# Kernel optimization log

Hardware: AMD Instinct MI355X
Metric: run time of the kernel (lower is better)

Reference implementation:

```python
import jax, jax.numpy as jnp
import numpy as np


def _conv(x, w, b, pad_h=0):
    # x: [B,C,H,W_feat], w: [O,C,kh,1]; kernel width is 1 so this is a 1D conv along H
    y = jax.lax.conv_general_dilated(
        x, w, window_strides=(1, 1), padding=[(pad_h, pad_h), (0, 0)],
        dimension_numbers=('NCHW', 'OIHW', 'NCHW'))
    return y + b[None, :, None, None]


def _lin(x, w, b):
    # Semi_Linear: shared nn.Linear applied to the last axis of every [channel, height] slice.
    # Since the nested loops cover the full leading dims, this is one batched matmul.
    return jnp.einsum('bchi,oi->bcho', x, w) + b


def setup_inputs() -> dict:
    key = jax.random.key(0)
    ks = jax.random.split(key, 40)
    B = 4096
    rn = lambda k, shape, s=0.1: jax.random.normal(k, shape, jnp.float32) * s
    d = {}
    d['x'] = jax.random.normal(ks[0], (B, 1, 5, 127), jnp.float32)
    # block A params (first set of definitions in __init__)
    d['ca1_w'] = rn(ks[1], (5, 1, 3, 1));    d['ca1_b'] = rn(ks[2], (5,))
    d['l01_w'] = rn(ks[3], (81, 127));        d['l01_b'] = rn(ks[4], (81,))
    d['cb1_w'] = rn(ks[5], (25, 5, 3, 1));    d['cb1_b'] = rn(ks[6], (25,))
    d['cc1_w'] = rn(ks[7], (25, 1, 1, 1));    d['cc1_b'] = rn(ks[8], (25,))
    d['r01_w'] = rn(ks[9], (81, 127));        d['r01_b'] = rn(ks[10], (81,))
    # block B params
    d['c1_w'] = rn(ks[11], (75, 25, 2, 1));   d['c1_b'] = rn(ks[12], (75,))
    d['l1_w'] = rn(ks[13], (30, 81));         d['l1_b'] = rn(ks[14], (30,))
    d['c2_w'] = rn(ks[15], (125, 75, 2, 1));  d['c2_b'] = rn(ks[16], (125,))
    d['ca_w'] = rn(ks[17], (125, 25, 3, 1));  d['ca_b'] = rn(ks[18], (125,))
    d['ra_w'] = rn(ks[19], (30, 81));         d['ra_b'] = rn(ks[20], (30,))
    # block C params (second, overriding set of definitions)
    d['ca2_w'] = rn(ks[21], (25, 125, 2, 1)); d['ca2_b'] = rn(ks[22], (25,))
    d['l02_w'] = rn(ks[23], (10, 30));        d['l02_b'] = rn(ks[24], (10,))
    d['cb2_w'] = rn(ks[25], (1, 25, 2, 1));   d['cb2_b'] = rn(ks[26], (1,))
    d['cc2_w'] = rn(ks[27], (1, 125, 1, 1));  d['cc2_b'] = rn(ks[28], (1,))
    d['r02_w'] = rn(ks[29], (10, 30));        d['r02_b'] = rn(ks[30], (10,))
    d['fl_w'] = rn(ks[31], (1, 10));          d['fl_b'] = rn(ks[32], (1,))
    return d


def reference(x, ca1_w, ca1_b, l01_w, l01_b, cb1_w, cb1_b, cc1_w, cc1_b, r01_w, r01_b,
              c1_w, c1_b, l1_w, l1_b, c2_w, c2_b, ca_w, ca_b, ra_w, ra_b,
              ca2_w, ca2_b, l02_w, l02_b, cb2_w, cb2_b, cc2_w, cc2_b, r02_w, r02_b,
              fl_w, fl_b):
    # block A
    z = _conv(x, ca1_w, ca1_b, pad_h=1)            # [B,5,5,127]
    z = jax.nn.relu(_lin(z, l01_w, l01_b))         # [B,5,5,81]
    z = _conv(z, cb1_w, cb1_b, pad_h=1)            # [B,25,5,81]
    y = _lin(x, r01_w, r01_b)                      # [B,1,5,81]
    y = _conv(y, cc1_w, cc1_b)                     # [B,25,5,81]
    x1 = z + y
    # block B
    z = _conv(x1, c1_w, c1_b)                      # [B,75,4,81]
    z = jax.nn.relu(_lin(z, l1_w, l1_b))           # [B,75,4,30]
    z = _conv(z, c2_w, c2_b)                       # [B,125,3,30]
    y = _lin(x1, ra_w, ra_b)                       # [B,25,5,30]
    y = _conv(y, ca_w, ca_b)                       # [B,125,3,30]
    x2 = z + y
    # block C
    z = _conv(x2, ca2_w, ca2_b)                    # [B,25,2,30]
    z = jax.nn.relu(_lin(z, l02_w, l02_b))         # [B,25,2,10]
    z = _conv(z, cb2_w, cb2_b)                     # [B,1,1,10]
    y = _lin(x2, r02_w, r02_b)                     # [B,125,3,10]
    y = _conv(y, cc2_w, cc2_b)                     # [B,1,3,10]
    x3 = z + y                                     # broadcast -> [B,1,3,10]
    return _lin(x3, fl_w, fl_b)                    # [B,1,3,1]
```

## Files before the change

### kernel.cpp

```cpp
#include <hip/hip_runtime.h>


typedef unsigned short u16;
typedef __attribute__((ext_vector_type(8))) short bf16x8;
typedef __attribute__((ext_vector_type(4))) float f32x4;
typedef __attribute__((ext_vector_type(8))) unsigned short u16x8;
typedef __attribute__((ext_vector_type(2))) unsigned int u32x2;

__device__ __forceinline__ float bf2f(u16 u) {
  return __uint_as_float(((unsigned)u) << 16);
}
__device__ __forceinline__ u16 f2bf(float f) {
  unsigned u = __float_as_uint(f);
  return (u16)((u + 0x7FFFu + ((u >> 16) & 1u)) >> 16);
}

#define Z4 make_float4(0.f, 0.f, 0.f, 0.f)

#define OF_CS01   0
#define OF_CS1    81
#define OF_CSR    111
#define OF_CSAC   141
#define OF_CS02   266
#define OF_CSCC2  276
#define OF_L01T   280
#define OF_R01T   10948
#define OF_SWT    21616
#define OF_CB1T   26800
#define OF_C1T    27175
#define OF_SCT    30928
#define OF_CA2T   31528
#define OF_WT2    41528
#define OF_ZPAD   57912
#define OF_C1W2   57920
#define F32_TOTAL 60480

#define R_XT   0
#define R_XL   635
#define R_YA   1040
#define R_ZA   1445
#define R_P    3470
#define R_Q    4970
#define R_VLP  5270
#define R_VRP  12770
#define R_TP   16520
#define R_X2   0
#define R_XJ   12770
#define ROWS_TOTAL 25520

struct Ctx {
  const float *x, *ca1_w, *ca1_b, *l01_b, *r01_b, *cb1_b, *cc1_w, *cc1_b;
  const float *c1_b, *l1_b, *c2_b, *ca_b, *ra_b, *ca2_b, *l02_b;
  const float *cb2_w, *cb2_b, *cc2_w, *cc2_b, *r02_b, *fl_w, *fl_b;
  const float *l01_w, *r01_w, *l1_w, *ra_w, *c1_w, *c2_w, *ca_w, *cb1_w;
  const float *l02_w, *r02_w, *ca2_w;
  float *F;
  float *zAcc;
  float *yAcc;
  u16 *A;
  float *out;
  int CB;
  int b0g;
};

__global__ __launch_bounds__(256) void k0c(Ctx C) {
  const int t0 = blockIdx.x * 256 + threadIdx.x;
  const int NT = 32 * 256;
  float* F = C.F;
  for (int k = t0; k < 277; k += NT) {
    float s = 0.f;
    if (k < 81)       { for (int i = 0; i < 127; ++i) s += C.l01_w[k * 127 + i]; F[OF_CS01 + k] = s; }
    else if (k < 111) { int j = k - 81;  for (int a = 0; a < 81; ++a) s += C.l1_w[j * 81 + a]; F[OF_CS1 + j] = s; }
    else if (k < 141) { int j = k - 111; for (int a = 0; a < 81; ++a) s += C.ra_w[j * 81 + a]; F[OF_CSR + j] = s; }
    else if (k < 266) { int o = k - 141; for (int i = 0; i < 75; ++i) s += C.ca_w[o * 75 + i]; F[OF_CSAC + o] = s; }
    else if (k < 276) { int q = k - 266; for (int j = 0; j < 30; ++j) s += C.l02_w[q * 30 + j]; F[OF_CS02 + q] = s; }
    else              { float ss = 0.f; for (int o = 0; o < 125; ++o) ss += C.cc2_w[o]; F[OF_CSCC2] = ss; }
  }
  for (int e = t0; e < 8; e += NT) F[OF_ZPAD + e] = 0.f;
  for (int e = t0; e < 10668; e += NT) { int i = e / 84, a = e % 84;
    F[OF_L01T + e] = (a < 81) ? C.l01_w[a * 127 + i] : 0.f; }
  for (int e = t0; e < 10668; e += NT) { int i = e / 84, a = e % 84;
    F[OF_R01T + e] = (a < 81) ? C.r01_w[a * 127 + i] : 0.f; }
  for (int e = t0; e < 5184; e += NT)  { int a = e / 64, j2 = e % 64;
    F[OF_SWT + e] = (j2 < 30) ? C.l1_w[j2 * 81 + a]
                  : (j2 < 60) ? C.ra_w[(j2 - 30) * 81 + a] : 0.f; }
  for (int e = t0; e < 375; e += NT)   { int k = e / 25, c = e % 25; F[OF_CB1T + e] = C.cb1_w[c * 15 + k]; }
  for (int e = t0; e < 600; e += NT)   { int j = e / 20, q2 = e % 20;
    F[OF_SCT + e] = (q2 < 10) ? C.l02_w[q2 * 30 + j] : C.r02_w[(q2 - 10) * 30 + j]; }
  for (int e = t0; e < 10000; e += NT) { int k = e / 40, r = e % 40, cg = r / 8, i = r % 8;
    F[OF_CA2T + e] = (i < 5) ? C.ca2_w[(cg * 5 + i) * 250 + k] : 0.f; }
  u16* WT2 = (u16*)(F + OF_WT2);
  for (int e = t0; e < 32768; e += NT) {
    int o = e >> 8, k = e & 255;
    float v = 0.f;
    if (o < 125) {
      if (k < 150) v = C.c2_w[o * 150 + k];
      else if (k >= 160 && k < 235) v = C.ca_w[o * 75 + (k - 160)];
    }
    WT2[e] = f2bf(v);
  }
  u16* C1W2 = (u16*)(F + OF_C1W2);
  for (int e = t0; e < 5120; e += NT) {
    int o = e >> 6, k = e & 63;
    float v = (o < 75 && k < 50) ? C.c1_w[o * 50 + k] : 0.f;
    C1W2[e] = f2bf(v);
  }
}

__global__ __launch_bounds__(256) void k0t(Ctx C) {
  __shared__ float tile[64][65];
  const int tid = threadIdx.x;
  const int b0 = blockIdx.x * 64;
  const int i0 = blockIdx.y * 64;
  for (int e = tid; e < 64 * 64; e += 256) {
    int s = e >> 6, ii = e & 63, gi = i0 + ii;
    if (gi < 635) tile[s][ii] = C.x[(size_t)(C.b0g + b0 + s) * 635 + gi];
  }
  __syncthreads();
  const int lane = tid & 63, wv = tid >> 6;
  u16* xT = C.A + (size_t)R_XT * C.CB;
#pragma unroll
  for (int k = 0; k < 16; ++k) {
    int r = wv * 16 + k, gi = i0 + r;
    if (gi < 635) xT[(size_t)gi * C.CB + b0 + lane] = f2bf(tile[lane][r]);
  }
}

__global__ __launch_bounds__(256) void k1(Ctx C) {
  const int col = blockIdx.x * 256 + threadIdx.x;
  if (col >= C.CB) return;
  const int g = blockIdx.y, type = g / 15, r = g % 15, h = r / 3, a0 = (r % 3) * 28;
  const size_t cb = (size_t)C.CB;
  const u16* __restrict__ xT = C.A + (size_t)R_XT * cb;
  const float* __restrict__ wT = C.F + (type ? OF_R01T : OF_L01T) + a0;
  float4 A0=Z4,A1=Z4,A2=Z4,A3=Z4,A4=Z4,A5=Z4,A6=Z4;
  for (int i = 0; i < 127; ++i) {
    float xv = bf2f(xT[(size_t)(h * 127 + i) * cb + col]);
    const float4* __restrict__ W = (const float4*)(wT + i * 84);
#define K1F(Aq, P) { float4 w = W[P]; Aq.x += w.x*xv; Aq.y += w.y*xv; Aq.z += w.z*xv; Aq.w += w.w*xv; }
    K1F(A0,0) K1F(A1,1) K1F(A2,2) K1F(A3,3) K1F(A4,4) K1F(A5,5) K1F(A6,6)
#undef K1F
  }
  u16* dst = C.A + (size_t)(type ? R_YA : R_XL) * cb;
  auto wr = [&](int a, float v) {
    if (a < 81) {
      float rr = v + (type ? C.r01_b[a] : 0.f);
      dst[(size_t)(h * 81 + a) * cb + col] = f2bf(rr);
    }
  };
#define K1O(Aq, P) { wr(a0+4*P+0, Aq.x); wr(a0+4*P+1, Aq.y); wr(a0+4*P+2, Aq.z); wr(a0+4*P+3, Aq.w); }
  K1O(A0,0) K1O(A1,1) K1O(A2,2) K1O(A3,3) K1O(A4,4) K1O(A5,5) K1O(A6,6)
#undef K1O
}

__global__ __launch_bounds__(256) void k2(Ctx C) {
  const int col = blockIdx.x * 256 + threadIdx.x;
  if (col >= C.CB) return;
  const int g = blockIdx.y, c5 = g / 15, r = g % 15, h = r / 3, a0 = (r % 3) * 27;
  const u16* __restrict__ XL = C.A + (size_t)R_XL * C.CB;
  const float* __restrict__ F = C.F;
  float acc[27];
  float cb = C.ca1_b[c5];
#pragma unroll
  for (int a = 0; a < 27; ++a) acc[a] = cb * F[OF_CS01 + a0 + a] + C.l01_b[a0 + a];
#pragma unroll
  for (int dh = 0; dh < 3; ++dh) {
    int hp = h - 1 + dh;
    if (hp < 0 || hp > 4) continue;
    float w = C.ca1_w[c5 * 3 + dh];
#pragma unroll
    for (int a = 0; a < 27; ++a) acc[a] += w * bf2f(XL[(size_t)(hp * 81 + a0 + a) * C.CB + col]);
  }
  u16* zA = C.A + (size_t)R_ZA * C.CB;
#pragma unroll
  for (int a = 0; a < 27; ++a)
    zA[(size_t)((c5 * 5 + h) * 81 + a0 + a) * C.CB + col] = f2bf(fmaxf(acc[a], 0.f));
}

__global__ __launch_bounds__(256) void k3(Ctx C) {
  const int col = blockIdx.x * 256 + threadIdx.x;
  if (col >= C.CB) return;
  const int g = blockIdx.y, pair = g >> 1, j0 = (g & 1) * 32;
  const bool isP = (pair < 25);
  const size_t cb = (size_t)C.CB;
  const u16* __restrict__ src = C.A + (size_t)(isP ? (R_ZA + pair * 81) : (R_YA + (pair - 25) * 81)) * cb;
  const float* __restrict__ SWT = C.F + OF_SWT + j0;
  float4 A0=Z4,A1=Z4,A2=Z4,A3=Z4,A4=Z4,A5=Z4,A6=Z4,A7=Z4;
  for (int a = 0; a < 81; ++a) {
    float xv = bf2f(src[(size_t)a * cb + col]);
    const float4* __restrict__ W = (const float4*)(SWT + a * 64);
#define K3F(Aq, P) { float4 w = W[P]; Aq.x += w.x*xv; Aq.y += w.y*xv; Aq.z += w.z*xv; Aq.w += w.w*xv; }
    K3F(A0,0) K3F(A1,1) K3F(A2,2) K3F(A3,3) K3F(A4,4) K3F(A5,5) K3F(A6,6) K3F(A7,7)
#undef K3F
  }
  u16* dst = C.A + (size_t)(isP ? (R_P + pair * 60) : (R_Q + (pair - 25) * 60)) * cb;
  auto wr = [&](int j2, float v) {
    if (j2 < 60) dst[(size_t)j2 * cb + col] = f2bf(v);
  };
#define K3O(Aq, P) { wr(j0+4*P+0, Aq.x); wr(j0+4*P+1, Aq.y); wr(j0+4*P+2, Aq.z); wr(j0+4*P+3, Aq.w); }
  K3O(A0,0) K3O(A1,1) K3O(A2,2) K3O(A3,3) K3O(A4,4) K3O(A5,5) K3O(A6,6) K3O(A7,7)
#undef K3O
}

__global__ __launch_bounds__(256) void k4(Ctx C) {
  const int col = blockIdx.x * 256 + threadIdx.x;
  if (col >= C.CB) return;
  const int g = blockIdx.y, cg = g / 60, j2 = g % 60;
  const size_t cb = (size_t)C.CB;
  const u16* __restrict__ Pb = C.A + (size_t)R_P * cb;
  const u16* __restrict__ Qb = C.A + (size_t)R_Q * cb;
  const float* __restrict__ F = C.F;
  float sj = (j2 < 30) ? F[OF_CS1 + j2] : F[OF_CSR + (j2 - 30)];
  float acc[5][5];
#pragma unroll
  for (int cl = 0; cl < 5; ++cl) {
    int c = cg * 5 + cl;
    float base = (C.cb1_b[c] + C.cc1_b[c]) * sj;
    float cw = C.cc1_w[c];
#pragma unroll
    for (int h = 0; h < 5; ++h)
      acc[cl][h] = base + cw * bf2f(Qb[(size_t)(h * 60 + j2) * cb + col]);
  }
#pragma unroll
  for (int c5 = 0; c5 < 5; ++c5)
#pragma unroll
    for (int hp = 0; hp < 5; ++hp) {
      float pv = bf2f(Pb[(size_t)((c5 * 5 + hp) * 60 + j2) * cb + col]);
#pragma unroll
      for (int dh = 0; dh < 3; ++dh) {
        int h = hp + 1 - dh;
        if (h < 0 || h > 4) continue;
        const float* __restrict__ w = F + OF_CB1T + (c5 * 3 + dh) * 25 + cg * 5;
#pragma unroll
        for (int cl = 0; cl < 5; ++cl) acc[cl][h] += w[cl] * pv;
      }
    }
  if (j2 < 30) {
    u16* vlp = C.A + (size_t)R_VLP * cb;
#pragma unroll
    for (int cl = 0; cl < 5; ++cl) {
      int base = (cg * 5 + cl) * 30 + j2;
#pragma unroll
      for (int h = 0; h < 5; ++h)
        vlp[(size_t)(base + h * 750) * cb + col] = f2bf(acc[cl][h]);
    }
  } else {
    u16* vrp = C.A + (size_t)R_VRP * cb;
    int jr = j2 - 30;
#pragma unroll
    for (int cl = 0; cl < 5; ++cl) {
      int base = (cg * 5 + cl) * 30 + jr;
#pragma unroll
      for (int h = 0; h < 5; ++h)
        vrp[(size_t)(base + h * 750) * cb + col] = f2bf(acc[cl][h]);
    }
  }
}

union CvtAF { u32x2 p[2]; bf16x8 v; };

__global__ __launch_bounds__(256, 2) void k5m(Ctx C) {
  __shared__ u16 sA[8192];
  const int tid = threadIdx.x;
  const int col0 = blockIdx.x * 128;
  const int gy = blockIdx.y;
  const int j = gy >> 2, h4 = gy & 3;
  const size_t cb = (size_t)C.CB;
  const u16* __restrict__ A_ = C.A;
  const u16* __restrict__ WB = (const u16*)(C.F + OF_C1W2);
  const float* __restrict__ F = C.F;

  const int x = tid & 63, wv = tid >> 6;
  const int klane = (x >> 1) & 3;
  const int m0s = ((x >> 3) << 4) + ((x & 1) << 3);
  const u16* zsrc = (const u16*)(F + OF_ZPAD);
#pragma unroll
  for (int p = 0; p < 4; ++p) {
    int k = p * 16 + wv * 4 + klane;
    const u16* src;
    if (k >= 50) {
      src = zsrc;
    } else {
      int c = k >> 1, dc = k & 1;
      int srow = R_VLP + (h4 + dc) * 750 + c * 30 + j;
      src = A_ + (size_t)srow * cb + col0 + m0s;
    }
    __builtin_amdgcn_global_load_lds(
        (const __attribute__((address_space(1))) void*)src,
        (__attribute__((address_space(3))) void*)&sA[(p * 4 + wv) * 512],
        16, 0, 0);
  }

  const int l = tid & 63, w = tid >> 6;
  const int lc = l & 15, q = l >> 4;
#define BF(N, S) (*(const bf16x8*)(WB + (size_t)((N)*16 + lc) * 64 + (S)*32 + q*8))
  bf16x8 B00 = BF(0,0), B10 = BF(1,0), B20 = BF(2,0), B30 = BF(3,0), B40 = BF(4,0);
  bf16x8 B01 = BF(0,1), B11 = BF(1,1), B21 = BF(2,1), B31 = BF(3,1), B41 = BF(4,1);
#undef BF
  float s1 = F[OF_CS1 + j], lb = C.l1_b[j];
  const int o4r = 64 + lc;
  const int o4c = (o4r < 75) ? o4r : 0;
  float bs0 = C.c1_b[lc] * s1 + lb;
  float bs1 = C.c1_b[16 + lc] * s1 + lb;
  float bs2 = C.c1_b[32 + lc] * s1 + lb;
  float bs3 = C.c1_b[48 + lc] * s1 + lb;
  float bs4 = C.c1_b[o4c] * s1 + lb;

  __syncthreads();

  unsigned ldsbase = (unsigned)(size_t)(&sA[0]);
  unsigned ta = ldsbase + (unsigned)((2 * q) * 1024 + w * 256 + lc * 8);

  u32x2 e00,e01,e02,e03, e10,e11,e12,e13;
  asm volatile("ds_read_b64_tr_b16 %0, %1"             : "=&v"(e00) : "v"(ta));
  asm volatile("ds_read_b64_tr_b16 %0, %1 offset:1024" : "=&v"(e01) : "v"(ta));
  asm volatile("ds_read_b64_tr_b16 %0, %1 offset:8192" : "=&v"(e02) : "v"(ta));
  asm volatile("ds_read_b64_tr_b16 %0, %1 offset:9216" : "=&v"(e03) : "v"(ta));
  asm volatile("ds_read_b64_tr_b16 %0, %1 offset:128"  : "=&v"(e10) : "v"(ta));
  asm volatile("ds_read_b64_tr_b16 %0, %1 offset:1152" : "=&v"(e11) : "v"(ta));
  asm volatile("ds_read_b64_tr_b16 %0, %1 offset:8320" : "=&v"(e12) : "v"(ta));
  asm volatile("ds_read_b64_tr_b16 %0, %1 offset:9344" : "=&v"(e13) : "v"(ta));
  asm volatile("s_waitcnt lgkmcnt(0)" ::: "memory");
  __builtin_amdgcn_sched_barrier(0);

  bf16x8 f0s0, f0s1, f1s0, f1s1;
  { CvtAF c_; c_.p[0]=e00; c_.p[1]=e01; f0s0=c_.v; }
  { CvtAF c_; c_.p[0]=e02; c_.p[1]=e03; f0s1=c_.v; }
  { CvtAF c_; c_.p[0]=e10; c_.p[1]=e11; f1s0=c_.v; }
  { CvtAF c_; c_.p[0]=e12; c_.p[1]=e13; f1s1=c_.v; }

  f32x4 a00={0,0,0,0},a01={0,0,0,0},a02={0,0,0,0},a03={0,0,0,0},a04={0,0,0,0};
  f32x4 a10={0,0,0,0},a11={0,0,0,0},a12={0,0,0,0},a13={0,0,0,0},a14={0,0,0,0};
#define MF(AC, FA, BB) AC = __builtin_amdgcn_mfma_f32_16x16x32_bf16(FA, BB, AC, 0, 0, 0);
  MF(a00,f0s0,B00) MF(a01,f0s0,B10) MF(a02,f0s0,B20) MF(a03,f0s0,B30) MF(a04,f0s0,B40)
  MF(a10,f1s0,B00) MF(a11,f1s0,B10) MF(a12,f1s0,B20) MF(a13,f1s0,B30) MF(a14,f1s0,B40)
  MF(a00,f0s1,B01) MF(a01,f0s1,B11) MF(a02,f0s1,B21) MF(a03,f0s1,B31) MF(a04,f0s1,B41)
  MF(a10,f1s1,B01) MF(a11,f1s1,B11) MF(a12,f1s1,B21) MF(a13,f1s1,B31) MF(a14,f1s1,B41)
#undef MF

  u16* tp = C.A + (size_t)R_TP * cb;
  const int cw0 = col0 + 2 * w * 16 + q * 4;
#define ST(AC, O, BS, CW) { int o_ = (O); if (o_ < 75) { \
    size_t rw = (size_t)(h4 * 2250 + o_ * 30 + j) * cb + (CW); \
    ushort4 pk; pk.x = f2bf(fmaxf(AC[0]+(BS),0.f)); pk.y = f2bf(fmaxf(AC[1]+(BS),0.f)); \
    pk.z = f2bf(fmaxf(AC[2]+(BS),0.f)); pk.w = f2bf(fmaxf(AC[3]+(BS),0.f)); \
    *(ushort4*)(tp + rw) = pk; } }
  ST(a00, lc,      bs0, cw0)      ST(a01, 16 + lc, bs1, cw0)
  ST(a02, 32 + lc, bs2, cw0)      ST(a03, 48 + lc, bs3, cw0)
  ST(a04, 64 + lc, bs4, cw0)
  ST(a10, lc,      bs0, cw0 + 16) ST(a11, 16 + lc, bs1, cw0 + 16)
  ST(a12, 32 + lc, bs2, cw0 + 16) ST(a13, 48 + lc, bs3, cw0 + 16)
  ST(a14, 64 + lc, bs4, cw0 + 16)
#undef ST
}

#define RD(D, TA, OFF) asm volatile("ds_read_b64_tr_b16 %0, %1 offset:" OFF : "=&v"(D) : "v"(TA));
#define TRS_EVEN(TA) \
  RD(p00,TA,"0")     RD(p01,TA,"1024")  RD(p10,TA,"8192")  RD(p11,TA,"9216") \
  RD(p20,TA,"16384") RD(p21,TA,"17408") RD(p30,TA,"24576") RD(p31,TA,"25600") \
  RD(p40,TA,"32768") RD(p41,TA,"33792") RD(p50,TA,"40960") RD(p51,TA,"41984") \
  RD(p60,TA,"49152") RD(p61,TA,"50176") RD(p70,TA,"57344") RD(p71,TA,"58368")
#define TRS_ODD(TA) \
  RD(p00,TA,"128")   RD(p01,TA,"1152")  RD(p10,TA,"8320")  RD(p11,TA,"9344") \
  RD(p20,TA,"16512") RD(p21,TA,"17536") RD(p30,TA,"24704") RD(p31,TA,"25728") \
  RD(p40,TA,"32896") RD(p41,TA,"33920") RD(p50,TA,"41088") RD(p51,TA,"42112") \
  RD(p60,TA,"49280") RD(p61,TA,"50304") RD(p70,TA,"57472") RD(p71,TA,"58496")

__global__ __launch_bounds__(256, 2) void k6m(Ctx C) {
  __shared__ u16 sA[32768];
  const int tid = threadIdx.x;
  const int col0 = blockIdx.x * 128;
  const int gy = blockIdx.y;
  const int j = gy / 3, h3 = gy % 3;
  const size_t cb = (size_t)C.CB;
  const u16* __restrict__ A_ = C.A;
  const u16* __restrict__ WT2 = (const u16*)(C.F + OF_WT2);
  const float* __restrict__ F = C.F;

  const int x = tid & 63, wv = tid >> 6;
  const int klane = (x >> 1) & 3;
  const int m0s = ((x >> 3) << 4) + ((x & 1) << 3);
  const u16* zsrc = (const u16*)(F + OF_ZPAD);
#pragma unroll
  for (int p = 0; p < 16; ++p) {
    int k = p * 16 + wv * 4 + klane;
    const u16* src;
    bool pad = (k >= 150 && k < 160) || (k >= 235);
    if (pad) {
      src = zsrc;
    } else {
      int srow;
      if (k < 150) srow = R_TP + (h3 + (k & 1)) * 2250 + (k >> 1) * 30 + j;
      else { int kk = k - 160; int c = kk / 3; srow = R_VRP + (h3 + (kk - c * 3)) * 750 + c * 30 + j; }
      src = A_ + (size_t)srow * cb + col0 + m0s;
    }
    __builtin_amdgcn_global_load_lds(
        (const __attribute__((address_space(1))) void*)src,
        (__attribute__((address_space(3))) void*)&sA[(p * 4 + wv) * 512],
        16, 0, 0);
  }

  const int l = tid & 63, w = tid >> 6;
  const int lc = l & 15, q = l >> 4;
  const u16* wbA = WT2 + (size_t)(w * 32 + lc) * 256 + q * 8;
  const u16* wbB = WT2 + (size_t)(w * 32 + 16 + lc) * 256 + q * 8;
  bf16x8 b00 = *(const bf16x8*)(wbA + 0*32), b01 = *(const bf16x8*)(wbA + 1*32),
         b02 = *(const bf16x8*)(wbA + 2*32), b03 = *(const bf16x8*)(wbA + 3*32),
         b04 = *(const bf16x8*)(wbA + 4*32), b05 = *(const bf16x8*)(wbA + 5*32),
         b06 = *(const bf16x8*)(wbA + 6*32), b07 = *(const bf16x8*)(wbA + 7*32);
  bf16x8 b10 = *(const bf16x8*)(wbB + 0*32), b11 = *(const bf16x8*)(wbB + 1*32),
         b12 = *(const bf16x8*)(wbB + 2*32), b13 = *(const bf16x8*)(wbB + 3*32),
         b14 = *(const bf16x8*)(wbB + 4*32), b15 = *(const bf16x8*)(wbB + 5*32),
         b16 = *(const bf16x8*)(wbB + 6*32), b17 = *(const bf16x8*)(wbB + 7*32);

  float rbj = C.ra_b[j];
  u16* x2b = C.A + (size_t)R_X2 * cb;
  const size_t rowbase = (size_t)(h3 * 30 + j) * 125;
  const int o0 = w * 32 + lc;
  const int o1 = o0 + 16;
  const int o1c = (o1 < 125) ? o1 : 0;
  float bs0 = C.c2_b[o0] + C.ca_b[o0] + rbj * F[OF_CSAC + o0];
  float bs1 = C.c2_b[o1c] + C.ca_b[o1c] + rbj * F[OF_CSAC + o1c];

  __syncthreads();

  unsigned ldsbase = (unsigned)(size_t)(&sA[0]);
  const unsigned ta0 = ldsbase + (unsigned)((2 * q) * 1024 + lc * 8);
  const unsigned ta1 = ta0 + 256;
  const unsigned ta2 = ta0 + 512;
  const unsigned ta3 = ta0 + 768;

  u32x2 p00,p01, p10,p11, p20,p21, p30,p31, p40,p41, p50,p51, p60,p61, p70,p71;

  TRS_EVEN(ta0)

#define MM(FS, BA, BB) \
    a0 = __builtin_amdgcn_mfma_f32_16x16x32_bf16(FS, BA, a0, 0, 0, 0); \
    a1 = __builtin_amdgcn_mfma_f32_16x16x32_bf16(FS, BB, a1, 0, 0, 0);

#define MG_BODY(MG, ...) { \
    asm volatile("s_waitcnt lgkmcnt(0)" ::: "memory"); \
    __builtin_amdgcn_sched_barrier(0); \
    bf16x8 f0,f1,f2,f3,f4,f5,f6,f7; \
    { CvtAF c_; c_.p[0]=p00; c_.p[1]=p01; f0=c_.v; } \
    { CvtAF c_; c_.p[0]=p10; c_.p[1]=p11; f1=c_.v; } \
    { CvtAF c_; c_.p[0]=p20; c_.p[1]=p21; f2=c_.v; } \
    { CvtAF c_; c_.p[0]=p30; c_.p[1]=p31; f3=c_.v; } \
    { CvtAF c_; c_.p[0]=p40; c_.p[1]=p41; f4=c_.v; } \
    { CvtAF c_; c_.p[0]=p50; c_.p[1]=p51; f5=c_.v; } \
    { CvtAF c_; c_.p[0]=p60; c_.p[1]=p61; f6=c_.v; } \
    { CvtAF c_; c_.p[0]=p70; c_.p[1]=p71; f7=c_.v; } \
    __VA_ARGS__ \
    f32x4 a0 = {0.f,0.f,0.f,0.f}, a1 = {0.f,0.f,0.f,0.f}; \
    MM(f0,b00,b10) MM(f1,b01,b11) MM(f2,b02,b12) MM(f3,b03,b13) \
    MM(f4,b04,b14) MM(f5,b05,b15) MM(f6,b06,b16) MM(f7,b07,b17) \
    const int cw = col0 + (MG) * 16 + q * 4; \
    { ushort4 pk; pk.x = f2bf(a0[0]+bs0); pk.y = f2bf(a0[1]+bs0); \
      pk.z = f2bf(a0[2]+bs0); pk.w = f2bf(a0[3]+bs0); \
      *(ushort4*)(x2b + (rowbase + o0) * cb + cw) = pk; } \
    if (o1 < 125) { ushort4 pk; pk.x = f2bf(a1[0]+bs1); pk.y = f2bf(a1[1]+bs1); \
      pk.z = f2bf(a1[2]+bs1); pk.w = f2bf(a1[3]+bs1); \
      *(ushort4*)(x2b + (rowbase + o1) * cb + cw) = pk; } \
  }

  MG_BODY(0, TRS_ODD(ta0))
  MG_BODY(1, TRS_EVEN(ta1))
  MG_BODY(2, TRS_ODD(ta1))
  MG_BODY(3, TRS_EVEN(ta2))
  MG_BODY(4, TRS_ODD(ta2))
  MG_BODY(5, TRS_EVEN(ta3))
  MG_BODY(6, TRS_ODD(ta3))
  MG_BODY(7)
#undef MG_BODY
#undef MM
}

__global__ __launch_bounds__(256) void k7(Ctx C) {
  const int col = blockIdx.x * 256 + threadIdx.x;
  if (col >= C.CB) return;
  const int g = blockIdx.y;
  const int o = g / 3, h3 = g % 3;
  const size_t cb = (size_t)C.CB;
  const u16* __restrict__ x2b = C.A + (size_t)R_X2 * cb;
  const float* __restrict__ SCT = C.F + OF_SCT;
  float4 A0=Z4,A1=Z4,A2=Z4,A3=Z4,A4=Z4;
  for (int j = 0; j < 30; ++j) {
    float xv = bf2f(x2b[(size_t)((h3 * 30 + j) * 125 + o) * cb + col]);
    const float4* __restrict__ W = (const float4*)(SCT + j * 20);
#define K7F(Aq, P) { float4 w = W[P]; Aq.x += w.x*xv; Aq.y += w.y*xv; Aq.z += w.z*xv; Aq.w += w.w*xv; }
    K7F(A0,0) K7F(A1,1) K7F(A2,2) K7F(A3,3) K7F(A4,4)
#undef K7F
  }
  u16* XJ = C.A + (size_t)R_XJ * cb;
  auto wq = [&](int qq, float v) { XJ[(size_t)(g * 10 + qq) * cb + col] = f2bf(v); };
  wq(0,A0.x); wq(1,A0.y); wq(2,A0.z); wq(3,A0.w);
  wq(4,A1.x); wq(5,A1.y); wq(6,A1.z); wq(7,A1.w);
  wq(8,A2.x); wq(9,A2.y);
  float s = C.fl_w[0]*A2.z + C.fl_w[1]*A2.w
          + C.fl_w[2]*A3.x + C.fl_w[3]*A3.y + C.fl_w[4]*A3.z + C.fl_w[5]*A3.w
          + C.fl_w[6]*A4.x + C.fl_w[7]*A4.y + C.fl_w[8]*A4.z + C.fl_w[9]*A4.w;
  atomicAdd(&C.yAcc[(size_t)h3 * C.CB + col], C.cc2_w[o] * s);
}

__global__ __launch_bounds__(256) void k8a(Ctx C) {
  const int col = blockIdx.x * 256 + threadIdx.x;
  if (col >= C.CB) return;
  const int g = blockIdx.y, cg = g / 20, rem = g % 20, hh = rem / 10, q = rem % 10;
  const size_t cb = (size_t)C.CB;
  const u16* __restrict__ XJ = C.A + (size_t)R_XJ * cb;
  const float* __restrict__ F = C.F;
  float4 A0 = Z4; float a4 = 0.f;
  const float* __restrict__ Wb = F + OF_CA2T + cg * 8;
  for (int k = 0; k < 250; ++k) {
    int o = k >> 1, dh = k & 1;
    float xv = bf2f(XJ[(size_t)((o * 3 + hh + dh) * 10 + q) * cb + col]);
    const float* __restrict__ wr = Wb + k * 40;
    float4 w0 = *(const float4*)wr;
    float w4 = wr[4];
    A0.x += w0.x * xv; A0.y += w0.y * xv; A0.z += w0.z * xv; A0.w += w0.w * xv;
    a4 += w4 * xv;
  }
  float s02 = F[OF_CS02 + q];
  float lb = C.l02_b[q];
  const int c0 = cg * 5;
  float part = 0.f;
  {
    float zc;
    zc = fmaxf(A0.x + C.ca2_b[c0+0] * s02 + lb, 0.f); part += C.cb2_w[(c0+0)*2+hh] * zc;
    zc = fmaxf(A0.y + C.ca2_b[c0+1] * s02 + lb, 0.f); part += C.cb2_w[(c0+1)*2+hh] * zc;
    zc = fmaxf(A0.z + C.ca2_b[c0+2] * s02 + lb, 0.f); part += C.cb2_w[(c0+2)*2+hh] * zc;
    zc = fmaxf(A0.w + C.ca2_b[c0+3] * s02 + lb, 0.f); part += C.cb2_w[(c0+3)*2+hh] * zc;
    zc = fmaxf(a4   + C.ca2_b[c0+4] * s02 + lb, 0.f); part += C.cb2_w[(c0+4)*2+hh] * zc;
  }
  atomicAdd(&C.zAcc[col], C.fl_w[q] * part);
}

__global__ __launch_bounds__(256) void k8c(Ctx C) {
  const int col = blockIdx.x * 256 + threadIdx.x;
  if (col >= C.CB) return;
  float scc2 = C.F[OF_CSCC2];
  float cst = C.fl_b[0];
#pragma unroll
  for (int q = 0; q < 10; ++q)
    cst += C.fl_w[q] * (C.cb2_b[0] + C.r02_b[q] * scc2 + C.cc2_b[0]);
  float za = C.zAcc[col];
#pragma unroll
  for (int h = 0; h < 3; ++h)
    C.out[(size_t)(C.b0g + col) * 3 + h] = cst + za + C.yAcc[(size_t)h * C.CB + col];
}

extern "C" void kernel_launch(void* const* d_in, const int* in_sizes, int n_in,
                              void* d_out, int out_size, void* d_ws, size_t ws_size,
                              hipStream_t stream) {
  (void)n_in; (void)out_size;
  Ctx C;
  C.x     = (const float*)d_in[0];
  C.ca1_w = (const float*)d_in[1];  C.ca1_b = (const float*)d_in[2];
  C.l01_w = (const float*)d_in[3];  C.l01_b = (const float*)d_in[4];
  C.cb1_w = (const float*)d_in[5];  C.cb1_b = (const float*)d_in[6];
  C.cc1_w = (const float*)d_in[7];  C.cc1_b = (const float*)d_in[8];
  C.r01_w = (const float*)d_in[9];  C.r01_b = (const float*)d_in[10];
  C.c1_w  = (const float*)d_in[11]; C.c1_b  = (const float*)d_in[12];
  C.l1_w  = (const float*)d_in[13]; C.l1_b  = (const float*)d_in[14];
  C.c2_w  = (const float*)d_in[15]; C.c2_b  = (const float*)d_in[16];
  C.ca_w  = (const float*)d_in[17]; C.ca_b  = (const float*)d_in[18];
  C.ra_w  = (const float*)d_in[19]; C.ra_b  = (const float*)d_in[20];
  C.ca2_w = (const float*)d_in[21]; C.ca2_b = (const float*)d_in[22];
  C.l02_w = (const float*)d_in[23]; C.l02_b = (const float*)d_in[24];
  C.cb2_w = (const float*)d_in[25]; C.cb2_b = (const float*)d_in[26];
  C.cc2_w = (const float*)d_in[27]; C.cc2_b = (const float*)d_in[28];
  C.r02_w = (const float*)d_in[29]; C.r02_b = (const float*)d_in[30];
  C.fl_w  = (const float*)d_in[31]; C.fl_b  = (const float*)d_in[32];
  C.out   = (float*)d_out;

  const int B = in_sizes[0] / 635;

  int CB = 4096;
  if (CB > B) CB = B;
  size_t accoff, actoff;
  for (;;) {
    accoff = ((size_t)F32_TOTAL * 4 + 255) & ~(size_t)255;
    actoff = (accoff + (size_t)4 * CB * 4 + 255) & ~(size_t)255;
    if (CB <= 256 || actoff + (size_t)ROWS_TOTAL * CB * 2 <= ws_size) break;
    CB >>= 1;
  }
  C.F = (float*)d_ws;
  C.zAcc = (float*)((char*)d_ws + accoff);
  C.yAcc = C.zAcc + CB;
  C.A = (u16*)((char*)d_ws + actoff);
  C.CB = CB;

  C.b0g = 0;
  k0c<<<dim3(32), dim3(256), 0, stream>>>(C);

  const int bt64 = CB / 64, bt128 = CB / 128, bt256 = (CB + 255) / 256;
  for (int b0 = 0; b0 < B; b0 += CB) {
    C.b0g = b0;
    hipMemsetAsync(C.zAcc, 0, (size_t)4 * CB * sizeof(float), stream);
    k0t<<<dim3(bt64, 10),   dim3(256), 0, stream>>>(C);
    k1 <<<dim3(bt256, 30),  dim3(256), 0, stream>>>(C);
    k2 <<<dim3(bt256, 75),  dim3(256), 0, stream>>>(C);
    k3 <<<dim3(bt256, 60),  dim3(256), 0, stream>>>(C);
    k4 <<<dim3(bt256, 300), dim3(256), 0, stream>>>(C);
    k5m<<<dim3(bt128, 120), dim3(256), 0, stream>>>(C);
    k6m<<<dim3(bt128, 90),  dim3(256), 0, stream>>>(C);
    k7 <<<dim3(bt256, 375), dim3(256), 0, stream>>>(C);
    k8a<<<dim3(bt256, 100), dim3(256), 0, stream>>>(C);
    k8c<<<dim3(bt256, 1),   dim3(256), 0, stream>>>(C);
  }
}
```

Measured before the change: 304.3 us.

## Split k6m K dimension into two LDS halves to raise occupancy

The k6m GEMM kernel now stages its 256-wide K operand in two halves of 128 through a 32 KB LDS buffer instead of loading all 64 KB at once, and loads weight fragments per half. Accumulators for all eight M-groups are held in registers across both halves, and occupancy hints rise from 2 to 3 blocks per CU. The aim is more resident blocks to hide global-to-LDS latency. The cost is an extra barrier round trip with no overlap between halves, plus more accumulator registers that may limit the higher occupancy.

```diff
diff --git a/kernel.cpp b/kernel.cpp
--- a/kernel.cpp
+++ b/kernel.cpp
@@ -355,19 +355,19 @@
 }
 
 #define RD(D, TA, OFF) asm volatile("ds_read_b64_tr_b16 %0, %1 offset:" OFF : "=&v"(D) : "v"(TA));
-#define TRS_EVEN(TA) \
-  RD(p00,TA,"0")     RD(p01,TA,"1024")  RD(p10,TA,"8192")  RD(p11,TA,"9216") \
-  RD(p20,TA,"16384") RD(p21,TA,"17408") RD(p30,TA,"24576") RD(p31,TA,"25600") \
-  RD(p40,TA,"32768") RD(p41,TA,"33792") RD(p50,TA,"40960") RD(p51,TA,"41984") \
-  RD(p60,TA,"49152") RD(p61,TA,"50176") RD(p70,TA,"57344") RD(p71,TA,"58368")
-#define TRS_ODD(TA) \
-  RD(p00,TA,"128")   RD(p01,TA,"1152")  RD(p10,TA,"8320")  RD(p11,TA,"9344") \
-  RD(p20,TA,"16512") RD(p21,TA,"17536") RD(p30,TA,"24704") RD(p31,TA,"25728") \
-  RD(p40,TA,"32896") RD(p41,TA,"33920") RD(p50,TA,"41088") RD(p51,TA,"42112") \
-  RD(p60,TA,"49280") RD(p61,TA,"50304") RD(p70,TA,"57472") RD(p71,TA,"58496")
-
-__global__ __launch_bounds__(256, 2) void k6m(Ctx C) {
-  __shared__ u16 sA[32768];
+#define TRS4_EVEN(TA) \
+  RD(p00,TA,"0")     RD(p01,TA,"1024") \
+  RD(p10,TA,"8192")  RD(p11,TA,"9216") \
+  RD(p20,TA,"16384") RD(p21,TA,"17408") \
+  RD(p30,TA,"24576") RD(p31,TA,"25600")
+#define TRS4_ODD(TA) \
+  RD(p00,TA,"128")   RD(p01,TA,"1152") \
+  RD(p10,TA,"8320")  RD(p11,TA,"9344") \
+  RD(p20,TA,"16512") RD(p21,TA,"17536") \
+  RD(p30,TA,"24704") RD(p31,TA,"25728")
+
+__global__ __launch_bounds__(256, 3) void k6m(Ctx C) {
+  __shared__ u16 sA[16384];
   const int tid = threadIdx.x;
   const int col0 = blockIdx.x * 128;
   const int gy = blockIdx.y;
@@ -381,37 +381,37 @@
   const int klane = (x >> 1) & 3;
   const int m0s = ((x >> 3) << 4) + ((x & 1) << 3);
   const u16* zsrc = (const u16*)(F + OF_ZPAD);
-#pragma unroll
-  for (int p = 0; p < 16; ++p) {
-    int k = p * 16 + wv * 4 + klane;
-    const u16* src;
-    bool pad = (k >= 150 && k < 160) || (k >= 235);
-    if (pad) {
-      src = zsrc;
-    } else {
-      int srow;
-      if (k < 150) srow = R_TP + (h3 + (k & 1)) * 2250 + (k >> 1) * 30 + j;
-      else { int kk = k - 160; int c = kk / 3; srow = R_VRP + (h3 + (kk - c * 3)) * 750 + c * 30 + j; }
-      src = A_ + (size_t)srow * cb + col0 + m0s;
-    }
-    __builtin_amdgcn_global_load_lds(
-        (const __attribute__((address_space(1))) void*)src,
-        (__attribute__((address_space(3))) void*)&sA[(p * 4 + wv) * 512],
-        16, 0, 0);
-  }
+
+#define STAGE(H) { \
+  _Pragma("unroll") \
+  for (int p = 0; p < 8; ++p) { \
+    int k = (H) * 128 + p * 16 + wv * 4 + klane; \
+    const u16* src; \
+    bool pad = (k >= 150 && k < 160) || (k >= 235); \
+    if (pad) { \
+      src = zsrc; \
+    } else { \
+      int srow; \
+      if (k < 150) srow = R_TP + (h3 + (k & 1)) * 2250 + (k >> 1) * 30 + j; \
+      else { int kk = k - 160; int c = kk / 3; srow = R_VRP + (h3 + (kk - c * 3)) * 750 + c * 30 + j; } \
+      src = A_ + (size_t)srow * cb + col0 + m0s; \
+    } \
+    __builtin_amdgcn_global_load_lds( \
+        (const __attribute__((address_space(1))) void*)src, \
+        (__attribute__((address_space(3))) void*)&sA[(p * 4 + wv) * 512], \
+        16, 0, 0); \
+  } }
 
   const int l = tid & 63, w = tid >> 6;
   const int lc = l & 15, q = l >> 4;
   const u16* wbA = WT2 + (size_t)(w * 32 + lc) * 256 + q * 8;
   const u16* wbB = WT2 + (size_t)(w * 32 + 16 + lc) * 256 + q * 8;
-  bf16x8 b00 = *(const bf16x8*)(wbA + 0*32), b01 = *(const bf16x8*)(wbA + 1*32),
-         b02 = *(const bf16x8*)(wbA + 2*32), b03 = *(const bf16x8*)(wbA + 3*32),
-         b04 = *(const bf16x8*)(wbA + 4*32), b05 = *(const bf16x8*)(wbA + 5*32),
-         b06 = *(const bf16x8*)(wbA + 6*32), b07 = *(const bf16x8*)(wbA + 7*32);
-  bf16x8 b10 = *(const bf16x8*)(wbB + 0*32), b11 = *(const bf16x8*)(wbB + 1*32),
-         b12 = *(const bf16x8*)(wbB + 2*32), b13 = *(const bf16x8*)(wbB + 3*32),
-         b14 = *(const bf16x8*)(wbB + 4*32), b15 = *(const bf16x8*)(wbB + 5*32),
-         b16 = *(const bf16x8*)(wbB + 6*32), b17 = *(const bf16x8*)(wbB + 7*32);
+  bf16x8 BA0, BA1, BA2, BA3, BB0, BB1, BB2, BB3;
+#define LOADB(H) { \
+    BA0 = *(const bf16x8*)(wbA + ((H)*4+0)*32); BA1 = *(const bf16x8*)(wbA + ((H)*4+1)*32); \
+    BA2 = *(const bf16x8*)(wbA + ((H)*4+2)*32); BA3 = *(const bf16x8*)(wbA + ((H)*4+3)*32); \
+    BB0 = *(const bf16x8*)(wbB + ((H)*4+0)*32); BB1 = *(const bf16x8*)(wbB + ((H)*4+1)*32); \
+    BB2 = *(const bf16x8*)(wbB + ((H)*4+2)*32); BB3 = *(const bf16x8*)(wbB + ((H)*4+3)*32); }
 
   float rbj = C.ra_b[j];
   u16* x2b = C.A + (size_t)R_X2 * cb;
@@ -422,57 +422,75 @@
   float bs0 = C.c2_b[o0] + C.ca_b[o0] + rbj * F[OF_CSAC + o0];
   float bs1 = C.c2_b[o1c] + C.ca_b[o1c] + rbj * F[OF_CSAC + o1c];
 
-  __syncthreads();
-
   unsigned ldsbase = (unsigned)(size_t)(&sA[0]);
   const unsigned ta0 = ldsbase + (unsigned)((2 * q) * 1024 + lc * 8);
   const unsigned ta1 = ta0 + 256;
   const unsigned ta2 = ta0 + 512;
   const unsigned ta3 = ta0 + 768;
 
-  u32x2 p00,p01, p10,p11, p20,p21, p30,p31, p40,p41, p50,p51, p60,p61, p70,p71;
-
-  TRS_EVEN(ta0)
-
-#define MM(FS, BA, BB) \
-    a0 = __builtin_amdgcn_mfma_f32_16x16x32_bf16(FS, BA, a0, 0, 0, 0); \
-    a1 = __builtin_amdgcn_mfma_f32_16x16x32_bf16(FS, BB, a1, 0, 0, 0);
-
-#define MG_BODY(MG, ...) { \
+  u32x2 p00,p01, p10,p11, p20,p21, p30,p31;
+  f32x4 cA0={0,0,0,0},cA1={0,0,0,0},cA2={0,0,0,0},cA3={0,0,0,0},
+        cA4={0,0,0,0},cA5={0,0,0,0},cA6={0,0,0,0},cA7={0,0,0,0},
+        cB0={0,0,0,0},cB1={0,0,0,0},cB2={0,0,0,0},cB3={0,0,0,0},
+        cB4={0,0,0,0},cB5={0,0,0,0},cB6={0,0,0,0},cB7={0,0,0,0};
+
+#define MGH(ACA, ACB, ...) { \
     asm volatile("s_waitcnt lgkmcnt(0)" ::: "memory"); \
     __builtin_amdgcn_sched_barrier(0); \
-    bf16x8 f0,f1,f2,f3,f4,f5,f6,f7; \
+    bf16x8 f0,f1,f2,f3; \
     { CvtAF c_; c_.p[0]=p00; c_.p[1]=p01; f0=c_.v; } \
     { CvtAF c_; c_.p[0]=p10; c_.p[1]=p11; f1=c_.v; } \
     { CvtAF c_; c_.p[0]=p20; c_.p[1]=p21; f2=c_.v; } \
     { CvtAF c_; c_.p[0]=p30; c_.p[1]=p31; f3=c_.v; } \
-    { CvtAF c_; c_.p[0]=p40; c_.p[1]=p41; f4=c_.v; } \
-    { CvtAF c_; c_.p[0]=p50; c_.p[1]=p51; f5=c_.v; } \
-    { CvtAF c_; c_.p[0]=p60; c_.p[1]=p61; f6=c_.v; } \
-    { CvtAF c_; c_.p[0]=p70; c_.p[1]=p71; f7=c_.v; } \
     __VA_ARGS__ \
-    f32x4 a0 = {0.f,0.f,0.f,0.f}, a1 = {0.f,0.f,0.f,0.f}; \
-    MM(f0,b00,b10) MM(f1,b01,b11) MM(f2,b02,b12) MM(f3,b03,b13) \
-    MM(f4,b04,b14) MM(f5,b05,b15) MM(f6,b06,b16) MM(f7,b07,b17) \
+    ACA = __builtin_amdgcn_mfma_f32_16x16x32_bf16(f0, BA0, ACA, 0, 0, 0); \
+    ACB = __builtin_amdgcn_mfma_f32_16x16x32_bf16(f0, BB0, ACB, 0, 0, 0); \
+    ACA = __builtin_amdgcn_mfma_f32_16x16x32_bf16(f1, BA1, ACA, 0, 0, 0); \
+    ACB = __builtin_amdgcn_mfma_f32_16x16x32_bf16(f1, BB1, ACB, 0, 0, 0); \
+    ACA = __builtin_amdgcn_mfma_f32_16x16x32_bf16(f2, BA2, ACA, 0, 0, 0); \
+    ACB = __builtin_amdgcn_mfma_f32_16x16x32_bf16(f2, BB2, ACB, 0, 0, 0); \
+    ACA = __builtin_amdgcn_mfma_f32_16x16x32_bf16(f3, BA3, ACA, 0, 0, 0); \
+    ACB = __builtin_amdgcn_mfma_f32_16x16x32_bf16(f3, BB3, ACB, 0, 0, 0); }
+
+#define STOREMG(MG, ACA, ACB) { \
     const int cw = col0 + (MG) * 16 + q * 4; \
-    { ushort4 pk; pk.x = f2bf(a0[0]+bs0); pk.y = f2bf(a0[1]+bs0); \
-      pk.z = f2bf(a0[2]+bs0); pk.w = f2bf(a0[3]+bs0); \
+    { ushort4 pk; pk.x = f2bf(ACA[0]+bs0); pk.y = f2bf(ACA[1]+bs0); \
+      pk.z = f2bf(ACA[2]+bs0); pk.w = f2bf(ACA[3]+bs0); \
       *(ushort4*)(x2b + (rowbase + o0) * cb + cw) = pk; } \
-    if (o1 < 125) { ushort4 pk; pk.x = f2bf(a1[0]+bs1); pk.y = f2bf(a1[1]+bs1); \
-      pk.z = f2bf(a1[2]+bs1); pk.w = f2bf(a1[3]+bs1); \
-      *(ushort4*)(x2b + (rowbase + o1) * cb + cw) = pk; } \
-  }
-
-  MG_BODY(0, TRS_ODD(ta0))
-  MG_BODY(1, TRS_EVEN(ta1))
-  MG_BODY(2, TRS_ODD(ta1))
-  MG_BODY(3, TRS_EVEN(ta2))
-  MG_BODY(4, TRS_ODD(ta2))
-  MG_BODY(5, TRS_EVEN(ta3))
-  MG_BODY(6, TRS_ODD(ta3))
-  MG_BODY(7)
-#undef MG_BODY
-#undef MM
+    if (o1 < 125) { ushort4 pk; pk.x = f2bf(ACB[0]+bs1); pk.y = f2bf(ACB[1]+bs1); \
+      pk.z = f2bf(ACB[2]+bs1); pk.w = f2bf(ACB[3]+bs1); \
+      *(ushort4*)(x2b + (rowbase + o1) * cb + cw) = pk; } }
+
+  STAGE(0)
+  LOADB(0)
+  __syncthreads();
+  TRS4_EVEN(ta0)
+  MGH(cA0, cB0, TRS4_ODD(ta0))
+  MGH(cA1, cB1, TRS4_EVEN(ta1))
+  MGH(cA2, cB2, TRS4_ODD(ta1))
+  MGH(cA3, cB3, TRS4_EVEN(ta2))
+  MGH(cA4, cB4, TRS4_ODD(ta2))
+  MGH(cA5, cB5, TRS4_EVEN(ta3))
+  MGH(cA6, cB6, TRS4_ODD(ta3))
+  MGH(cA7, cB7, )
+  __syncthreads();
+
+  STAGE(1)
+  LOADB(1)
+  __syncthreads();
+  TRS4_EVEN(ta0)
+  MGH(cA0, cB0, TRS4_ODD(ta0))   STOREMG(0, cA0, cB0)
+  MGH(cA1, cB1, TRS4_EVEN(ta1))  STOREMG(1, cA1, cB1)
+  MGH(cA2, cB2, TRS4_ODD(ta1))   STOREMG(2, cA2, cB2)
+  MGH(cA3, cB3, TRS4_EVEN(ta2))  STOREMG(3, cA3, cB3)
+  MGH(cA4, cB4, TRS4_ODD(ta2))   STOREMG(4, cA4, cB4)
+  MGH(cA5, cB5, TRS4_EVEN(ta3))  STOREMG(5, cA5, cB5)
+  MGH(cA6, cB6, TRS4_ODD(ta3))   STOREMG(6, cA6, cB6)
+  MGH(cA7, cB7, )                STOREMG(7, cA7, cB7)
+#undef MGH
+#undef STOREMG
+#undef LOADB
+#undef STAGE
 }
 
 __global__ __launch_bounds__(256) void k7(Ctx C) {
```

Measured after the change: 365.8 us. +20.2%, slower.
